# Optimization experiments

Hardware: AMD Instinct MI355X
Metric: run time of the kernel (lower is better)

## Reference

```python
import jax, jax.numpy as jnp
import numpy as np

N = 100000
E = 1600000
D = 128      # input feature dim
H = 128      # hidden_channels
O = 2        # out_channels
NEG_SLOPE = 0.2
EPS = 1e-16  # PyG softmax denominator epsilon


def gat_conv(x, src, dst, W_src, W_dst, att_src, att_dst, bias):
    """PyG GATConv, heads=1, add_self_loops=False, concat=True."""
    xs = x @ W_src                      # [N, C]
    xd = x @ W_dst                      # [N, C]
    a_s = xs @ att_src                  # [N]
    a_d = xd @ att_dst                  # [N]
    e = jax.nn.leaky_relu(a_s[src] + a_d[dst], NEG_SLOPE)   # [E]
    # segment softmax over edges grouped by destination node
    m = jax.ops.segment_max(e, dst, num_segments=N)          # [N]
    m = jnp.where(jnp.isfinite(m), m, 0.0)
    ex = jnp.exp(e - m[dst])                                  # [E]
    denom = jax.ops.segment_sum(ex, dst, num_segments=N)      # [N]
    alpha = ex / (denom[dst] + EPS)                            # [E]
    msg = alpha[:, None] * xs[src]                             # [E, C]
    out = jax.ops.segment_sum(msg, dst, num_segments=N)       # [N, C]
    return out + bias


def setup_inputs() -> dict:
    key = jax.random.key(0)
    ks = jax.random.split(key, 14)
    s = lambda k, shape, fan: jax.random.normal(k, shape, jnp.float32) * (1.0 / np.sqrt(fan))
    x = jax.random.normal(ks[0], (N, D), jnp.float32)
    edge_index = jax.random.randint(ks[1], (2, E), 0, N, dtype=jnp.int32)
    return {
        "x": x,
        "edge_index": edge_index,
        "W1s": s(ks[2], (D, H), D), "W1d": s(ks[3], (D, H), D),
        "a1s": s(ks[4], (H,), H),   "a1d": s(ks[5], (H,), H),
        "b1": jnp.zeros((H,), jnp.float32),
        "W2s": s(ks[6], (H, H), H), "W2d": s(ks[7], (H, H), H),
        "a2s": s(ks[8], (H,), H),   "a2d": s(ks[9], (H,), H),
        "b2": jnp.zeros((H,), jnp.float32),
        "Wl": s(ks[10], (H, O), H), "bl": jnp.zeros((O,), jnp.float32),
    }


def reference(x, edge_index, W1s, W1d, a1s, a1d, b1, W2s, W2d, a2s, a2d, b2, Wl, bl):
    src, dst = edge_index[0], edge_index[1]
    h = jax.nn.relu(gat_conv(x, src, dst, W1s, W1d, a1s, a1d, b1))
    # dropout p=0.3 is identity at inference
    h = jax.nn.relu(gat_conv(h, src, dst, W2s, W2d, a2s, a2d, b2))
    return h @ Wl + bl  # [N, O]
```

## Files before the change

### kernel.cpp

```cpp
#include <hip/hip_runtime.h>
#include <hip/hip_fp16.h>

#define NBSHIFT 8
#define BSZ     256
#define CAP     5120

typedef _Float16 f16x8 __attribute__((ext_vector_type(8)));
typedef float    f32x4 __attribute__((ext_vector_type(4)));


#define GEMM_LDS_BYTES (128 * 136 * 2 + 512)

__device__ __forceinline__ void gemm_body(
        const float* __restrict__ X, const float* __restrict__ Ws,
        const float* __restrict__ Wd, const float* __restrict__ attd,
        const float* __restrict__ att,
        __half* __restrict__ Y, float* __restrict__ a_s, float* __restrict__ a_d,
        int N, int blk, char* smem) {
    _Float16 (*sWh)[136] = (_Float16(*)[136])smem;
    float* svd = (float*)(smem + 128 * 136 * 2);
    int t = threadIdx.x;

    if (t < 128) {
        const float4* wr = (const float4*)&Wd[t * 128];
        const float4* ar = (const float4*)attd;
        float s = 0.f;
#pragma unroll 8
        for (int j = 0; j < 32; j++) {
            float4 w = wr[j], a = ar[j];
            s += w.x * a.x + w.y * a.y + w.z * a.z + w.w * a.w;
        }
        svd[t] = s;
    }
#pragma unroll
    for (int i = 0; i < 16; i++) {
        int gid = t + i * 256;
        int n = gid & 127, kq = gid >> 7;
        _Float16 p[4];
        p[0] = (_Float16)Ws[(kq * 4 + 0) * 128 + n];
        p[1] = (_Float16)Ws[(kq * 4 + 1) * 128 + n];
        p[2] = (_Float16)Ws[(kq * 4 + 2) * 128 + n];
        p[3] = (_Float16)Ws[(kq * 4 + 3) * 128 + n];
        *(uint2*)&sWh[n][kq * 4] = *(uint2*)p;
    }
    __syncthreads();

    int l = t & 63, wv = t >> 6;
    int quad = l >> 4, lm = l & 15;
    int rbase = blk * 64 + wv * 16;
    int arow = rbase + lm;
    bool rok = arow < N;
    const float* xrow = X + (size_t)arow * 128;

    f32x4 acc[8];
#pragma unroll
    for (int c = 0; c < 8; c++) acc[c] = (f32x4){0.f, 0.f, 0.f, 0.f};
    float adp = 0.f;

#pragma unroll
    for (int kc = 0; kc < 4; kc++) {
        int k0 = kc * 32 + quad * 8;
        float xf[8];
        if (rok) {
            *(float4*)&xf[0] = *(const float4*)&xrow[k0];
            *(float4*)&xf[4] = *(const float4*)&xrow[k0 + 4];
        } else {
#pragma unroll
            for (int j = 0; j < 8; j++) xf[j] = 0.f;
        }
        float4 v0 = *(const float4*)&svd[k0];
        float4 v1 = *(const float4*)&svd[k0 + 4];
        adp += xf[0] * v0.x + xf[1] * v0.y + xf[2] * v0.z + xf[3] * v0.w
             + xf[4] * v1.x + xf[5] * v1.y + xf[6] * v1.z + xf[7] * v1.w;
        f16x8 af;
#pragma unroll
        for (int j = 0; j < 8; j++) af[j] = (_Float16)xf[j];
#pragma unroll
        for (int c = 0; c < 8; c++) {
            f16x8 bf = *(const f16x8*)&sWh[c * 16 + lm][k0];
            acc[c] = __builtin_amdgcn_mfma_f32_16x16x32_f16(af, bf, acc[c], 0, 0, 0);
        }
    }

    adp += __shfl_xor(adp, 16);
    adp += __shfl_xor(adp, 32);
    if (quad == 0 && rok) a_d[arow] = adp;

    float attc[8];
#pragma unroll
    for (int c = 0; c < 8; c++) attc[c] = att[c * 16 + lm];
#pragma unroll
    for (int r = 0; r < 4; r++) {
        int grow = rbase + quad * 4 + r;
        bool gok = grow < N;
        float p = 0.f;
#pragma unroll
        for (int c = 0; c < 8; c++) {
            if (gok) Y[(size_t)grow * 128 + c * 16 + lm] = __float2half(acc[c][r]);
            p += acc[c][r] * attc[c];
        }
        p += __shfl_xor(p, 1); p += __shfl_xor(p, 2); p += __shfl_xor(p, 4); p += __shfl_xor(p, 8);
        if (lm == 0 && gok) a_s[grow] = p;
    }
}

__global__ __launch_bounds__(256, 4) void k_fuse1(
        const float* __restrict__ X, const float* __restrict__ W1s,
        const float* __restrict__ W1d, const float* __restrict__ a1d,
        const float* __restrict__ a1s,
        __half* __restrict__ Y, float* __restrict__ a_s, float* __restrict__ a_d, int N, int gb,
        const int* __restrict__ src, const int* __restrict__ dst, int E,
        int* __restrict__ cursor, unsigned* __restrict__ pairs) {
    __shared__ __align__(16) char smem[GEMM_LDS_BYTES];
    int t = threadIdx.x;

    if ((int)blockIdx.x >= gb) {
        int* hist  = (int*)smem;
        int* start = hist + 512;
        hist[t] = 0; hist[t + 256] = 0;
        __syncthreads();
        int e0 = (blockIdx.x - gb) * 1024 + t * 4;
        int d[4], s[4];
        bool full = (e0 + 3 < E);
        if (full) {
            int4 dv = *(const int4*)&dst[e0];
            int4 sv = *(const int4*)&src[e0];
            d[0] = dv.x; d[1] = dv.y; d[2] = dv.z; d[3] = dv.w;
            s[0] = sv.x; s[1] = sv.y; s[2] = sv.z; s[3] = sv.w;
#pragma unroll
            for (int i = 0; i < 4; i++) atomicAdd(&hist[d[i] >> NBSHIFT], 1);
        } else {
#pragma unroll
            for (int i = 0; i < 4; i++) {
                if (e0 + i < E) { d[i] = dst[e0 + i]; s[i] = src[e0 + i]; atomicAdd(&hist[d[i] >> NBSHIFT], 1); }
                else d[i] = -1;
            }
        }
        __syncthreads();
        if (hist[t] > 0)       start[t]       = atomicAdd(&cursor[t],       hist[t]);
        if (hist[t + 256] > 0) start[t + 256] = atomicAdd(&cursor[t + 256], hist[t + 256]);
        __syncthreads();
        hist[t] = 0; hist[t + 256] = 0;
        __syncthreads();
#pragma unroll
        for (int i = 0; i < 4; i++) {
            if (full || (e0 + i < E)) {
                int b = d[i] >> NBSHIFT;
                int r = atomicAdd(&hist[b], 1);
                pairs[b * CAP + start[b] + r] = ((unsigned)(d[i] & (BSZ - 1)) << 17) | (unsigned)s[i];
            }
        }
        return;
    }

    gemm_body(X, W1s, W1d, a1d, a1s, Y, a_s, a_d, N, blockIdx.x, smem);
}

__global__ __launch_bounds__(256, 4) void k_gemm2(
        const float* __restrict__ X, const float* __restrict__ W2s,
        const float* __restrict__ W2d, const float* __restrict__ a2d,
        const float* __restrict__ a2s,
        __half* __restrict__ Y, float* __restrict__ a_s, float* __restrict__ a_d, int N) {
    __shared__ __align__(16) char smem[GEMM_LDS_BYTES];
    gemm_body(X, W2s, W2d, a2d, a2s, Y, a_s, a_d, N, blockIdx.x, smem);
}

__global__ __launch_bounds__(256) void kB_csr(const unsigned* __restrict__ pairs,
                                              const int* __restrict__ cursor,
                                              int* __restrict__ row_start, int* __restrict__ row_end,
                                              int* __restrict__ csr_src, int N) {
    __shared__ int cnt[BSZ];
    __shared__ int cur[BSZ];
    __shared__ int sS[256];
    int b = blockIdx.x, t = threadIdx.x;
    int base = b * CAP;
    int ecnt = cursor[b];
    int nodeBase = b << NBSHIFT;
    cnt[t] = 0;
    __syncthreads();
    for (int j = t; j < ecnt; j += 256)
        atomicAdd(&cnt[pairs[base + j] >> 17], 1);
    __syncthreads();
    int c0 = cnt[t];
    sS[t] = c0; __syncthreads();
    for (int off = 1; off < 256; off <<= 1) {
        int x = (t >= off) ? sS[t - off] : 0;
        __syncthreads();
        sS[t] += x;
        __syncthreads();
    }
    int excl = sS[t] - c0;
    cur[t] = excl;
    int g = nodeBase + t;
    if (g < N) { row_start[g] = base + excl; row_end[g] = base + excl + c0; }
    __syncthreads();
    for (int j = t; j < ecnt; j += 256) {
        unsigned p = pairs[base + j];
        int r = atomicAdd(&cur[p >> 17], 1);
        csr_src[base + r] = (int)(p & 0x1FFFFu);
    }
}


template <bool HEAD>
__global__ __launch_bounds__(256) void k_agg(const int* __restrict__ csr_src, const int* __restrict__ row_start,
                                             const int* __restrict__ row_end,
                                             const float* __restrict__ a_s, const float* __restrict__ a_d,
                                             const __half* __restrict__ xs, const float* __restrict__ bias,
                                             const float* __restrict__ Wl, const float* __restrict__ bl,
                                             float* __restrict__ out, int N) {
    int t = threadIdx.x; int wv = t >> 6, l = t & 63;
    int n = blockIdx.x * 4 + wv;
    if (n >= N) return;
    int rs = row_start[n], re = row_end[n];
    int deg = re - rs;
    float adn = a_d[n];
    int q = l >> 4;
    int c = (l & 15) * 8;

    float aA[8], aB[8];
#pragma unroll
    for (int k = 0; k < 8; k++) { aA[k] = 0.f; aB[k] = 0.f; }
    float dn = 0.f;
    const int* cs = csr_src + rs;

    int i = q;
    for (; i + 4 < deg; i += 8) {
        int sA = cs[i];
        int sB = cs[i + 4];
        float tA = a_s[sA] + adn;
        float tB = a_s[sB] + adn;
        tA = tA > 0.f ? tA : 0.2f * tA;
        tB = tB > 0.f ? tB : 0.2f * tB;
        float exA = __expf(tA);
        float exB = __expf(tB);
        dn += exA + exB;
        uint4 uA = *(const uint4*)&xs[(size_t)sA * 128 + c];
        uint4 uB = *(const uint4*)&xs[(size_t)sB * 128 + c];
        const __half2* hA = (const __half2*)&uA;
        const __half2* hB = (const __half2*)&uB;
#pragma unroll
        for (int k = 0; k < 4; k++) {
            float2 fA = __half22float2(hA[k]);
            float2 fB = __half22float2(hB[k]);
            aA[2 * k] += exA * fA.x; aA[2 * k + 1] += exA * fA.y;
            aB[2 * k] += exB * fB.x; aB[2 * k + 1] += exB * fB.y;
        }
    }
    for (; i < deg; i += 4) {
        int s = cs[i];
        float tv = a_s[s] + adn;
        tv = tv > 0.f ? tv : 0.2f * tv;
        float ex = __expf(tv);
        dn += ex;
        uint4 u = *(const uint4*)&xs[(size_t)s * 128 + c];
        const __half2* h2 = (const __half2*)&u;
#pragma unroll
        for (int k = 0; k < 4; k++) {
            float2 f = __half22float2(h2[k]);
            aA[2 * k] += ex * f.x; aA[2 * k + 1] += ex * f.y;
        }
    }

    dn += __shfl_xor(dn, 16);
    dn += __shfl_xor(dn, 32);
    float inv = 1.f / (dn + 1e-16f);

    float hv[8];
    float4 b0 = *(const float4*)&bias[c];
    float4 b1 = *(const float4*)&bias[c + 4];
    float bb[8] = {b0.x, b0.y, b0.z, b0.w, b1.x, b1.y, b1.z, b1.w};
#pragma unroll
    for (int k = 0; k < 8; k++) {
        float v = aA[k] + aB[k];
        v += __shfl_xor(v, 16);
        v += __shfl_xor(v, 32);
        v = v * inv + bb[k];
        hv[k] = v > 0.f ? v : 0.f;
    }

    if (HEAD) {
        float p0 = 0.f, p1 = 0.f;
#pragma unroll
        for (int k = 0; k < 8; k++) {
            p0 += hv[k] * Wl[2 * (c + k)];
            p1 += hv[k] * Wl[2 * (c + k) + 1];
        }
#pragma unroll
        for (int o = 8; o > 0; o >>= 1) { p0 += __shfl_xor(p0, o); p1 += __shfl_xor(p1, o); }
        if (l == 0) { out[2 * n] = p0 + bl[0]; out[2 * n + 1] = p1 + bl[1]; }
    } else {
        if (q == 0) {
            *(float4*)&out[(size_t)n * 128 + c]     = make_float4(hv[0], hv[1], hv[2], hv[3]);
            *(float4*)&out[(size_t)n * 128 + c + 4] = make_float4(hv[4], hv[5], hv[6], hv[7]);
        }
    }
}


extern "C" void kernel_launch(void* const* d_in, const int* in_sizes, int n_in,
                              void* d_out, int out_size, void* d_ws, size_t ws_size,
                              hipStream_t stream) {
    const float* x   = (const float*)d_in[0];
    const int*   ei  = (const int*)d_in[1];
    const float* W1s = (const float*)d_in[2];
    const float* W1d = (const float*)d_in[3];
    const float* a1s = (const float*)d_in[4];
    const float* a1d = (const float*)d_in[5];
    const float* b1  = (const float*)d_in[6];
    const float* W2s = (const float*)d_in[7];
    const float* W2d = (const float*)d_in[8];
    const float* a2s = (const float*)d_in[9];
    const float* a2d = (const float*)d_in[10];
    const float* b2  = (const float*)d_in[11];
    const float* Wl  = (const float*)d_in[12];
    const float* bl  = (const float*)d_in[13];
    float* out = (float*)d_out;

    int N = in_sizes[0] / 128;
    int E = in_sizes[1] / 2;
    const int* srcA = ei;
    const int* dstA = ei + E;
    int NB = (N + BSZ - 1) >> NBSHIFT;

    __half* xs = (__half*)d_ws;
    float* h   = (float*)(xs + (size_t)N * 128);
    float* as_ = h + (size_t)N * 128;
    float* ad_ = as_ + N;
    int* row_start = (int*)(ad_ + N);
    int* row_end   = row_start + N;
    int* csr_src   = row_end + N;
    int* cursor    = csr_src + (size_t)NB * CAP;
    unsigned* pairs = (unsigned*)h;

    int gb = (N + 63) / 64;
    int EB = (E + 1023) / 1024;
    int ab = (N + 3) / 4;

    hipMemsetAsync(cursor, 0, (size_t)NB * 4, stream);

    k_fuse1<<<gb + EB, 256, 0, stream>>>(x, W1s, W1d, a1d, a1s, xs, as_, ad_, N, gb,
                                         srcA, dstA, E, cursor, pairs);

    kB_csr<<<NB, 256, 0, stream>>>(pairs, cursor, row_start, row_end, csr_src, N);

    k_agg<false><<<ab, 256, 0, stream>>>(csr_src, row_start, row_end, as_, ad_, xs, b1, nullptr, nullptr, h, N);

    k_gemm2<<<gb, 256, 0, stream>>>(h, W2s, W2d, a2d, a2s, xs, as_, ad_, N);

    k_agg<true><<<ab, 256, 0, stream>>>(csr_src, row_start, row_end, as_, ad_, xs, b2, Wl, bl, out, N);
}
```

Measured before the change: 336.9 us.

## Store layer-1 hidden in fp16 and share edge weights across the wave via shuffles

The first aggregation now writes its hidden output as fp16 instead of fp32, and the second GEMM reads fp16 input directly. This halves the write and read traffic for the intermediate tensor. The aggregation loop is also reworked: each chunk of 64 edges has its indices loaded and attention weights computed once per lane, then broadcast with shuffles, and the feature gathers are unrolled four-wide. Before, each edge's weight and exp were recomputed by all 16 lanes of a quad. The trade-off is lower precision in the hidden features and in the a_d dot product, plus extra shuffle instructions.

Result: no change. 334.5 us (-0.7%).

```diff
diff --git a/kernel.cpp b/kernel.cpp
--- a/kernel.cpp
+++ b/kernel.cpp
@@ -11,8 +11,9 @@
 
 #define GEMM_LDS_BYTES (128 * 136 * 2 + 512)
 
+template <bool XHALF>
 __device__ __forceinline__ void gemm_body(
-        const float* __restrict__ X, const float* __restrict__ Ws,
+        const void* __restrict__ Xv, const float* __restrict__ Ws,
         const float* __restrict__ Wd, const float* __restrict__ attd,
         const float* __restrict__ att,
         __half* __restrict__ Y, float* __restrict__ a_s, float* __restrict__ a_d,
@@ -50,7 +51,6 @@
     int rbase = blk * 64 + wv * 16;
     int arow = rbase + lm;
     bool rok = arow < N;
-    const float* xrow = X + (size_t)arow * 128;
 
     f32x4 acc[8];
 #pragma unroll
@@ -61,20 +61,33 @@
     for (int kc = 0; kc < 4; kc++) {
         int k0 = kc * 32 + quad * 8;
         float xf[8];
-        if (rok) {
-            *(float4*)&xf[0] = *(const float4*)&xrow[k0];
-            *(float4*)&xf[4] = *(const float4*)&xrow[k0 + 4];
+        f16x8 af;
+        if constexpr (XHALF) {
+            const __half* xrow = (const __half*)Xv + (size_t)arow * 128;
+            if (rok) {
+                af = *(const f16x8*)&xrow[k0];
+            } else {
+#pragma unroll
+                for (int j = 0; j < 8; j++) af[j] = (_Float16)0.f;
+            }
+#pragma unroll
+            for (int j = 0; j < 8; j++) xf[j] = (float)af[j];
         } else {
-#pragma unroll
-            for (int j = 0; j < 8; j++) xf[j] = 0.f;
+            const float* xrow = (const float*)Xv + (size_t)arow * 128;
+            if (rok) {
+                *(float4*)&xf[0] = *(const float4*)&xrow[k0];
+                *(float4*)&xf[4] = *(const float4*)&xrow[k0 + 4];
+            } else {
+#pragma unroll
+                for (int j = 0; j < 8; j++) xf[j] = 0.f;
+            }
+#pragma unroll
+            for (int j = 0; j < 8; j++) af[j] = (_Float16)xf[j];
         }
         float4 v0 = *(const float4*)&svd[k0];
         float4 v1 = *(const float4*)&svd[k0 + 4];
         adp += xf[0] * v0.x + xf[1] * v0.y + xf[2] * v0.z + xf[3] * v0.w
              + xf[4] * v1.x + xf[5] * v1.y + xf[6] * v1.z + xf[7] * v1.w;
-        f16x8 af;
-#pragma unroll
-        for (int j = 0; j < 8; j++) af[j] = (_Float16)xf[j];
 #pragma unroll
         for (int c = 0; c < 8; c++) {
             f16x8 bf = *(const f16x8*)&sWh[c * 16 + lm][k0];
@@ -153,16 +166,16 @@
         return;
     }
 
-    gemm_body(X, W1s, W1d, a1d, a1s, Y, a_s, a_d, N, blockIdx.x, smem);
+    gemm_body<false>(X, W1s, W1d, a1d, a1s, Y, a_s, a_d, N, blockIdx.x, smem);
 }
 
 __global__ __launch_bounds__(256, 4) void k_gemm2(
-        const float* __restrict__ X, const float* __restrict__ W2s,
+        const __half* __restrict__ X, const float* __restrict__ W2s,
         const float* __restrict__ W2d, const float* __restrict__ a2d,
         const float* __restrict__ a2s,
         __half* __restrict__ Y, float* __restrict__ a_s, float* __restrict__ a_d, int N) {
     __shared__ __align__(16) char smem[GEMM_LDS_BYTES];
-    gemm_body(X, W2s, W2d, a2d, a2s, Y, a_s, a_d, N, blockIdx.x, smem);
+    gemm_body<true>(X, W2s, W2d, a2d, a2s, Y, a_s, a_d, N, blockIdx.x, smem);
 }
 
 __global__ __launch_bounds__(256) void kB_csr(const unsigned* __restrict__ pairs,
@@ -202,13 +215,23 @@
 }
 
 
+#define ACC_EDGE(u, wj)  do {                                   \
+    const __half2* _h2 = (const __half2*)&(u);                  \
+    _Pragma("unroll")                                           \
+    for (int _k = 0; _k < 4; _k++) {                            \
+        float2 _f = __half22float2(_h2[_k]);                    \
+        acc[2 * _k]     += (wj) * _f.x;                         \
+        acc[2 * _k + 1] += (wj) * _f.y;                         \
+    }                                                           \
+} while (0)
+
 template <bool HEAD>
 __global__ __launch_bounds__(256) void k_agg(const int* __restrict__ csr_src, const int* __restrict__ row_start,
                                              const int* __restrict__ row_end,
                                              const float* __restrict__ a_s, const float* __restrict__ a_d,
                                              const __half* __restrict__ xs, const float* __restrict__ bias,
                                              const float* __restrict__ Wl, const float* __restrict__ bl,
-                                             float* __restrict__ out, int N) {
+                                             void* __restrict__ outv, int N) {
     int t = threadIdx.x; int wv = t >> 6, l = t & 63;
     int n = blockIdx.x * 4 + wv;
     if (n >= N) return;
@@ -217,54 +240,61 @@
     float adn = a_d[n];
     int q = l >> 4;
     int c = (l & 15) * 8;
-
-    float aA[8], aB[8];
-#pragma unroll
-    for (int k = 0; k < 8; k++) { aA[k] = 0.f; aB[k] = 0.f; }
-    float dn = 0.f;
     const int* cs = csr_src + rs;
 
-    int i = q;
-    for (; i + 4 < deg; i += 8) {
-        int sA = cs[i];
-        int sB = cs[i + 4];
-        float tA = a_s[sA] + adn;
-        float tB = a_s[sB] + adn;
-        tA = tA > 0.f ? tA : 0.2f * tA;
-        tB = tB > 0.f ? tB : 0.2f * tB;
-        float exA = __expf(tA);
-        float exB = __expf(tB);
-        dn += exA + exB;
-        uint4 uA = *(const uint4*)&xs[(size_t)sA * 128 + c];
-        uint4 uB = *(const uint4*)&xs[(size_t)sB * 128 + c];
-        const __half2* hA = (const __half2*)&uA;
-        const __half2* hB = (const __half2*)&uB;
-#pragma unroll
-        for (int k = 0; k < 4; k++) {
-            float2 fA = __half22float2(hA[k]);
-            float2 fB = __half22float2(hB[k]);
-            aA[2 * k] += exA * fA.x; aA[2 * k + 1] += exA * fA.y;
-            aB[2 * k] += exB * fB.x; aB[2 * k + 1] += exB * fB.y;
-        }
-    }
-    for (; i < deg; i += 4) {
-        int s = cs[i];
-        float tv = a_s[s] + adn;
-        tv = tv > 0.f ? tv : 0.2f * tv;
-        float ex = __expf(tv);
-        dn += ex;
-        uint4 u = *(const uint4*)&xs[(size_t)s * 128 + c];
-        const __half2* h2 = (const __half2*)&u;
-#pragma unroll
-        for (int k = 0; k < 4; k++) {
-            float2 f = __half22float2(h2[k]);
-            aA[2 * k] += ex * f.x; aA[2 * k + 1] += ex * f.y;
-        }
-    }
-
-    dn += __shfl_xor(dn, 16);
-    dn += __shfl_xor(dn, 32);
-    float inv = 1.f / (dn + 1e-16f);
+    float acc[8];
+#pragma unroll
+    for (int k = 0; k < 8; k++) acc[k] = 0.f;
+    float dnl = 0.f;
+
+    for (int base = 0; base < deg; base += 64) {
+        int m = deg - base; if (m > 64) m = 64;
+        int idx = 0; float w = 0.f;
+        if (l < m) {
+            idx = cs[base + l];
+            float tv = a_s[idx] + adn;
+            tv = tv > 0.f ? tv : 0.2f * tv;
+            w = __expf(tv);
+        }
+        dnl += w;
+        int mc = (m + 3) & ~3;
+        int e = q;
+        for (; e + 12 < mc; e += 16) {
+            int   s0 = __shfl(idx, e);      float w0 = __shfl(w, e);
+            int   s1 = __shfl(idx, e + 4);  float w1 = __shfl(w, e + 4);
+            int   s2 = __shfl(idx, e + 8);  float w2 = __shfl(w, e + 8);
+            int   s3 = __shfl(idx, e + 12); float w3 = __shfl(w, e + 12);
+            uint4 u0 = *(const uint4*)&xs[(size_t)s0 * 128 + c];
+            uint4 u1 = *(const uint4*)&xs[(size_t)s1 * 128 + c];
+            uint4 u2 = *(const uint4*)&xs[(size_t)s2 * 128 + c];
+            uint4 u3 = *(const uint4*)&xs[(size_t)s3 * 128 + c];
+            ACC_EDGE(u0, w0);
+            ACC_EDGE(u1, w1);
+            ACC_EDGE(u2, w2);
+            ACC_EDGE(u3, w3);
+        }
+        for (; e + 4 < mc; e += 8) {
+            int   s0 = __shfl(idx, e);      float w0 = __shfl(w, e);
+            int   s1 = __shfl(idx, e + 4);  float w1 = __shfl(w, e + 4);
+            uint4 u0 = *(const uint4*)&xs[(size_t)s0 * 128 + c];
+            uint4 u1 = *(const uint4*)&xs[(size_t)s1 * 128 + c];
+            ACC_EDGE(u0, w0);
+            ACC_EDGE(u1, w1);
+        }
+        for (; e < mc; e += 4) {
+            int   s0 = __shfl(idx, e);      float w0 = __shfl(w, e);
+            uint4 u0 = *(const uint4*)&xs[(size_t)s0 * 128 + c];
+            ACC_EDGE(u0, w0);
+        }
+    }
+
+    dnl += __shfl_xor(dnl, 1);
+    dnl += __shfl_xor(dnl, 2);
+    dnl += __shfl_xor(dnl, 4);
+    dnl += __shfl_xor(dnl, 8);
+    dnl += __shfl_xor(dnl, 16);
+    dnl += __shfl_xor(dnl, 32);
+    float inv = 1.f / (dnl + 1e-16f);
 
     float hv[8];
     float4 b0 = *(const float4*)&bias[c];
@@ -272,7 +302,7 @@
     float bb[8] = {b0.x, b0.y, b0.z, b0.w, b1.x, b1.y, b1.z, b1.w};
 #pragma unroll
     for (int k = 0; k < 8; k++) {
-        float v = aA[k] + aB[k];
+        float v = acc[k];
         v += __shfl_xor(v, 16);
         v += __shfl_xor(v, 32);
         v = v * inv + bb[k];
@@ -288,11 +318,15 @@
         }
 #pragma unroll
         for (int o = 8; o > 0; o >>= 1) { p0 += __shfl_xor(p0, o); p1 += __shfl_xor(p1, o); }
+        float* out = (float*)outv;
         if (l == 0) { out[2 * n] = p0 + bl[0]; out[2 * n + 1] = p1 + bl[1]; }
     } else {
         if (q == 0) {
-            *(float4*)&out[(size_t)n * 128 + c]     = make_float4(hv[0], hv[1], hv[2], hv[3]);
-            *(float4*)&out[(size_t)n * 128 + c + 4] = make_float4(hv[4], hv[5], hv[6], hv[7]);
+            __half* hout = (__half*)outv;
+            __half hb[8];
+#pragma unroll
+            for (int k = 0; k < 8; k++) hb[k] = __float2half(hv[k]);
+            *(uint4*)&hout[(size_t)n * 128 + c] = *(uint4*)hb;
         }
     }
 }
@@ -324,8 +358,8 @@
     int NB = (N + BSZ - 1) >> NBSHIFT;
 
     __half* xs = (__half*)d_ws;
-    float* h   = (float*)(xs + (size_t)N * 128);
-    float* as_ = h + (size_t)N * 128;
+    __half* h  = xs + (size_t)N * 128;
+    float* as_ = (float*)(h + (size_t)N * 128);
     float* ad_ = as_ + N;
     int* row_start = (int*)(ad_ + N);
     int* row_end   = row_start + N;
```
